# Performance work log

Hardware: AMD Instinct MI355X
Metric: run time of the kernel (lower is better)

Reference implementation:

```python
import jax, jax.numpy as jnp
import numpy as np

N = 50000        # nodes
E = 800000       # edges
D_IN = 128       # input feature dim
HID = 64         # hidden_dim
HEADS = 4
OUT = 2          # output_dim (fraud / not-fraud)
BN_EPS = 1e-5
NEG_SLOPE = 0.2  # PyG GATv2Conv default


def setup_inputs() -> dict:
    key = jax.random.key(0)
    ks = jax.random.split(key, 16)
    g = lambda k, shape, s=0.05: (jax.random.normal(k, shape, jnp.float32) * s)
    HC = HEADS * HID  # 256
    return {
        "x": jax.random.normal(ks[0], (N, D_IN), jnp.float32),
        "edge_index": jax.random.randint(ks[1], (2, E), 0, N),
        # input projection
        "W_in": g(ks[2], (D_IN, HID)), "b_in": jnp.zeros((HID,), jnp.float32),
        # GATv2 layer 0: HID -> HID, 4 heads (concat -> 256)
        "Wl0": g(ks[3], (HID, HC)), "Wr0": g(ks[4], (HID, HC)),
        "att0": g(ks[5], (HEADS, HID)), "bias0": jnp.zeros((HC,), jnp.float32),
        # GATv2 layer 1: 256 -> HID, 4 heads (concat -> 256)
        "Wl1": g(ks[6], (HC, HC)), "Wr1": g(ks[7], (HC, HC)),
        "att1": g(ks[8], (HEADS, HID)), "bias1": jnp.zeros((HC,), jnp.float32),
        # GATv2 layer 2: 256 -> OUT, 1 head
        "Wl2": g(ks[9], (HC, OUT)), "Wr2": g(ks[10], (HC, OUT)),
        "att2": g(ks[11], (1, OUT)), "bias2": jnp.zeros((OUT,), jnp.float32),
        # BatchNorm (eval mode: running stats) for the first num_layers-1 = 2 layers
        "bn_gamma": jnp.ones((2, HC), jnp.float32),
        "bn_beta": jnp.zeros((2, HC), jnp.float32),
        "bn_mean": jnp.zeros((2, HC), jnp.float32),
        "bn_var": jnp.ones((2, HC), jnp.float32),
    }


def _gatv2(h, src, dst, Wl, Wr, att, bias):
    """PyG GATv2Conv (concat=True, negative_slope=0.2). src->dst messages."""
    n = h.shape[0]
    heads, c = att.shape
    xl = (h @ Wl).reshape(n, heads, c)   # source transform
    xr = (h @ Wr).reshape(n, heads, c)   # target transform
    e = jax.nn.leaky_relu(xl[src] + xr[dst], NEG_SLOPE)       # [E, H, C]
    logits = jnp.einsum('ehc,hc->eh', e, att)                 # [E, H]
    # segment softmax over incoming edges of each destination node
    m = jax.ops.segment_max(logits, dst, num_segments=n)      # [N, H]
    ex = jnp.exp(logits - m[dst])
    denom = jax.ops.segment_sum(ex, dst, num_segments=n)
    alpha = ex / denom[dst]                                   # [E, H]
    out = jax.ops.segment_sum(xl[src] * alpha[..., None], dst, num_segments=n)
    return out.reshape(n, heads * c) + bias


def _bn_eval(h, gamma, beta, mean, var):
    return gamma * (h - mean) * jax.lax.rsqrt(var + BN_EPS) + beta


def reference(x, edge_index, W_in, b_in, Wl0, Wr0, att0, bias0,
              Wl1, Wr1, att1, bias1, Wl2, Wr2, att2, bias2,
              bn_gamma, bn_beta, bn_mean, bn_var):
    n = x.shape[0]
    loop = jnp.arange(n)
    src = jnp.concatenate([edge_index[0], loop])  # PyG add_self_loops=True
    dst = jnp.concatenate([edge_index[1], loop])

    h = jax.nn.relu(x @ W_in + b_in)              # dropout is identity in eval

    # layer 0 (no residual: 64 != 256)
    h = _gatv2(h, src, dst, Wl0, Wr0, att0, bias0)
    h = jax.nn.relu(_bn_eval(h, bn_gamma[0], bn_beta[0], bn_mean[0], bn_var[0]))

    # layer 1 (residual: 256 == 256)
    h_prev = h
    h = _gatv2(h, src, dst, Wl1, Wr1, att1, bias1)
    h = jax.nn.relu(_bn_eval(h, bn_gamma[1], bn_beta[1], bn_mean[1], bn_var[1]))
    h = h + h_prev

    # output layer, 1 head
    h = _gatv2(h, src, dst, Wl2, Wr2, att2, bias2)
    return jax.nn.log_softmax(h, axis=1)
```

## Files before the change

kernel.cpp:

```cpp
#include <hip/hip_runtime.h>
#include <hip/hip_bf16.h>
#include <math.h>


using h16     = _Float16;
using half2v  = __attribute__((ext_vector_type(2))) h16;
using half4v  = __attribute__((ext_vector_type(4))) h16;
using half8   = __attribute__((ext_vector_type(8))) h16;
using floatx4 = __attribute__((ext_vector_type(4))) float;

__device__ __forceinline__ float lrelu(float x) { return x > 0.f ? x : 0.2f * x; }

__device__ __forceinline__ half2v shfl_xor_h2(half2v v, int mask) {
    float f = __builtin_bit_cast(float, v);
    f = __shfl_xor(f, mask, 64);
    return __builtin_bit_cast(half2v, f);
}

__global__ void zero_int(int* __restrict__ p, int n) {
    int t = blockIdx.x * blockDim.x + threadIdx.x;
    if (t < n) p[t] = 0;
}

__global__ void hist_dst(const int* __restrict__ ei, int E, int* __restrict__ deg) {
    int e = blockIdx.x * blockDim.x + threadIdx.x;
    if (e < E) atomicAdd(&deg[ei[E + e]], 1);
}

__global__ __launch_bounds__(256) void scan_blk(const int* __restrict__ deg,
                                                int* __restrict__ rowstart,
                                                int* __restrict__ bsum, int N) {
    int t = blockIdx.x * 256 + threadIdx.x;
    int lane = threadIdx.x & 63, wid = threadIdx.x >> 6;
    int v = (t < N) ? deg[t] : 0;
    int x = v;
#pragma unroll
    for (int off = 1; off < 64; off <<= 1) {
        int y = __shfl_up(x, off, 64);
        if (lane >= off) x += y;
    }
    __shared__ int wsum[4];
    if (lane == 63) wsum[wid] = x;
    __syncthreads();
    int add = 0;
#pragma unroll
    for (int w = 0; w < 4; ++w) if (w < wid) add += wsum[w];
    int incl = x + add;
    if (t < N) rowstart[t] = incl - v;
    if (threadIdx.x == 255) bsum[blockIdx.x] = incl;
}

__global__ __launch_bounds__(256) void scan_off(int* __restrict__ bsum, int NB) {
    int t = threadIdx.x;
    int lane = t & 63, wid = t >> 6;
    int v = (t < NB) ? bsum[t] : 0;
    int x = v;
#pragma unroll
    for (int off = 1; off < 64; off <<= 1) {
        int y = __shfl_up(x, off, 64);
        if (lane >= off) x += y;
    }
    __shared__ int wsum[4];
    if (lane == 63) wsum[wid] = x;
    __syncthreads();
    int add = 0;
#pragma unroll
    for (int w = 0; w < 4; ++w) if (w < wid) add += wsum[w];
    if (t < NB) bsum[t] = x + add - v;
}

__global__ void add_off(const int* __restrict__ bsum, int* __restrict__ rowstart,
                        int* __restrict__ cursor, int N) {
    int t = blockIdx.x * 256 + threadIdx.x;
    if (t >= N) return;
    int r = rowstart[t] + bsum[blockIdx.x];
    rowstart[t] = r;
    cursor[t] = r;
}

__global__ void scatter_src(const int* __restrict__ ei, int E,
                            int* __restrict__ cursor, int* __restrict__ csr_src) {
    int e = blockIdx.x * blockDim.x + threadIdx.x;
    if (e >= E) return;
    int d = ei[E + e];
    int pos = atomicAdd(&cursor[d], 1);
    csr_src[pos] = ei[e];
}

__device__ __forceinline__ void pack_one(const float* __restrict__ W,
                                         h16* __restrict__ Wp,
                                         int t, int K, int NC) {
    int j = t & 7;
    int l = (t >> 3) & 63;
    int rest = t >> 9;
    int NT = NC >> 4;
    int nt = rest % NT;
    int kc = rest / NT;
    int row = kc * 32 + (l >> 4) * 8 + j;
    int col = nt * 16 + (l & 15);
    Wp[t] = (h16)W[(size_t)row * NC + col];
}

__global__ void pack_all(const float* __restrict__ W_in,
                         const float* __restrict__ Wl0, const float* __restrict__ Wr0,
                         const float* __restrict__ Wl1, const float* __restrict__ Wr1,
                         h16* __restrict__ P_in,
                         h16* __restrict__ P_l0, h16* __restrict__ P_r0,
                         h16* __restrict__ P_l1, h16* __restrict__ P_r1,
                         const float4* __restrict__ x, half4v* __restrict__ xh, int n4) {
    int t = blockIdx.x * blockDim.x + threadIdx.x;
    if (t < 8192)        pack_one(W_in, P_in, t, 128, 64);
    else if (t < 24576)  pack_one(Wl0, P_l0, t - 8192, 64, 256);
    else if (t < 40960)  pack_one(Wr0, P_r0, t - 24576, 64, 256);
    else if (t < 106496) pack_one(Wl1, P_l1, t - 40960, 256, 256);
    else if (t < 172032) pack_one(Wr1, P_r1, t - 106496, 256, 256);
    else {
        int u = t - 172032;
        if (u < n4) {
            float4 v = x[u];
            half4v o = { (h16)v.x, (h16)v.y, (h16)v.z, (h16)v.w };
            xh[u] = o;
        }
    }
}

template<int KC, int NT, bool RELU, bool DUAL>
__global__ __launch_bounds__(256) void gemm_lds(
        const h16* __restrict__ Xh,
        const h16* __restrict__ Wp0, const h16* __restrict__ Wp1,
        const float* __restrict__ bias,
        h16* __restrict__ out0, h16* __restrict__ out1, int M) {
    constexpr int K = KC * 32;
    constexpr int ldo = NT * 16;
    constexpr int CHUNK8 = NT * 64;
    constexpr int PER_THR = CHUNK8 / 256;
    __shared__ half8 wbuf[2][CHUNK8];

    const h16* Wp = (DUAL && blockIdx.y) ? Wp1 : Wp0;
    h16* out = (DUAL && blockIdx.y) ? out1 : out0;
    const half8* WG = (const half8*)Wp;

    const int tid = threadIdx.x;
    const int wid = tid >> 6, lane = tid & 63;
    const int quad = lane >> 4, li = lane & 15;
    const int r0 = blockIdx.x * 64 + wid * 16;
    int arow = r0 + li; if (arow >= M) arow = M - 1;
    const half8* A8 = (const half8*)Xh + (size_t)arow * (K / 8) + quad;

    floatx4 acc[NT];
#pragma unroll
    for (int t = 0; t < NT; ++t) acc[t] = (floatx4){0.f, 0.f, 0.f, 0.f};

    half8 st[PER_THR];
#pragma unroll
    for (int i = 0; i < PER_THR; ++i) st[i] = WG[i * 256 + tid];
#pragma unroll
    for (int i = 0; i < PER_THR; ++i) wbuf[0][i * 256 + tid] = st[i];
    __syncthreads();

#pragma unroll
    for (int kc = 0; kc < KC; ++kc) {
        int cur = kc & 1;
        if (kc + 1 < KC) {
#pragma unroll
            for (int i = 0; i < PER_THR; ++i)
                st[i] = WG[(size_t)(kc + 1) * CHUNK8 + i * 256 + tid];
        }
        half8 a = A8[kc * 4];
#pragma unroll
        for (int nt = 0; nt < NT; ++nt) {
            half8 b = wbuf[cur][nt * 64 + lane];
            acc[nt] = __builtin_amdgcn_mfma_f32_16x16x32_f16(a, b, acc[nt], 0, 0, 0);
        }
        if (kc + 1 < KC) {
#pragma unroll
            for (int i = 0; i < PER_THR; ++i) wbuf[cur ^ 1][i * 256 + tid] = st[i];
        }
        __syncthreads();
    }

#pragma unroll
    for (int nt = 0; nt < NT; ++nt) {
#pragma unroll
        for (int reg = 0; reg < 4; ++reg) {
            int rr = r0 + quad * 4 + reg;
            if (rr >= M) continue;
            float v = acc[nt][reg];
            if (RELU) v = fmaxf(v + bias[nt * 16 + li], 0.f);
            out[(size_t)rr * ldo + nt * 16 + li] = (h16)v;
        }
    }
}

__global__ void attn4_bn(int N, const h16* __restrict__ XL, const h16* __restrict__ XR,
                         const float* __restrict__ att,
                         const int* __restrict__ rowstart, const int* __restrict__ deg,
                         const int* __restrict__ csr_src,
                         const float* __restrict__ gamma, const float* __restrict__ beta,
                         const float* __restrict__ mean, const float* __restrict__ var,
                         const float* __restrict__ bias, const float* __restrict__ resid,
                         float* __restrict__ out, h16* __restrict__ outb) {
    int d = blockIdx.x * (blockDim.x >> 6) + (threadIdx.x >> 6);
    int lane = threadIdx.x & 63;
    if (d >= N) return;
    half4v bv = *(const half4v*)(XR + (size_t)d * 256 + lane * 4);
    float4 wf = ((const float4*)att)[lane];
    half2v b0 = bv.xy, b1 = bv.zw;
    half2v w0 = { (h16)wf.x, (h16)wf.y };
    half2v w1 = { (h16)wf.z, (h16)wf.w };
    const h16 k02 = (h16)0.2f;

    auto edge_part = [&](half4v xv) -> h16 {
        half2v e0 = xv.xy + b0, e1 = xv.zw + b1;
        half2v l0 = __builtin_elementwise_max(e0, e0 * k02);
        half2v l1 = __builtin_elementwise_max(e1, e1 * k02);
        half2v qd = l0 * w0 + l1 * w1;
        return qd.x + qd.y;
    };

    half4v av = *(const half4v*)(XL + (size_t)d * 256 + lane * 4);
    float p = (float)edge_part(av);
    p += __shfl_xor(p, 1, 64); p += __shfl_xor(p, 2, 64);
    p += __shfl_xor(p, 4, 64); p += __shfl_xor(p, 8, 64);
    float es = __expf(p);
    float l = es;
    float4 acc = { es * (float)av.x, es * (float)av.y, es * (float)av.z, es * (float)av.w };

    int start = rowstart[d], n = deg[d];
    for (int i = 0; i < n; i += 4) {
        int nm1 = n - 1;
        int s0 = csr_src[start + i];
        int s1 = csr_src[start + min(i + 1, nm1)];
        int s2 = csr_src[start + min(i + 2, nm1)];
        int s3 = csr_src[start + min(i + 3, nm1)];
        half4v x0 = *(const half4v*)(XL + (size_t)s0 * 256 + lane * 4);
        half4v x1 = *(const half4v*)(XL + (size_t)s1 * 256 + lane * 4);
        half4v x2 = *(const half4v*)(XL + (size_t)s2 * 256 + lane * 4);
        half4v x3 = *(const half4v*)(XL + (size_t)s3 * 256 + lane * 4);
        half2v p01 = { edge_part(x0), edge_part(x1) };
        half2v p23 = { edge_part(x2), edge_part(x3) };
#pragma unroll
        for (int s = 1; s < 16; s <<= 1) {
            p01 += shfl_xor_h2(p01, s);
            p23 += shfl_xor_h2(p23, s);
        }
        int rem = n - i;
        float e0 = __expf((float)p01.x);
        float e1 = (rem > 1) ? __expf((float)p01.y) : 0.f;
        float e2 = (rem > 2) ? __expf((float)p23.x) : 0.f;
        float e3 = (rem > 3) ? __expf((float)p23.y) : 0.f;
        l += (e0 + e1) + (e2 + e3);
        acc.x += e0 * (float)x0.x + e1 * (float)x1.x + e2 * (float)x2.x + e3 * (float)x3.x;
        acc.y += e0 * (float)x0.y + e1 * (float)x1.y + e2 * (float)x2.y + e3 * (float)x3.y;
        acc.z += e0 * (float)x0.z + e1 * (float)x1.z + e2 * (float)x2.z + e3 * (float)x3.z;
        acc.w += e0 * (float)x0.w + e1 * (float)x1.w + e2 * (float)x2.w + e3 * (float)x3.w;
    }
    float inv = 1.f / l;
    float4 g  = ((const float4*)gamma)[lane];
    float4 be = ((const float4*)beta)[lane];
    float4 mu = ((const float4*)mean)[lane];
    float4 va = ((const float4*)var)[lane];
    float4 bi = ((const float4*)bias)[lane];
    float4 sc4, sh4;
    sc4.x = g.x * rsqrtf(va.x + 1e-5f); sh4.x = (bi.x - mu.x) * sc4.x + be.x;
    sc4.y = g.y * rsqrtf(va.y + 1e-5f); sh4.y = (bi.y - mu.y) * sc4.y + be.y;
    sc4.z = g.z * rsqrtf(va.z + 1e-5f); sh4.z = (bi.z - mu.z) * sc4.z + be.z;
    sc4.w = g.w * rsqrtf(va.w + 1e-5f); sh4.w = (bi.w - mu.w) * sc4.w + be.w;
    float4 o;
    o.x = fmaxf(acc.x * inv * sc4.x + sh4.x, 0.f);
    o.y = fmaxf(acc.y * inv * sc4.y + sh4.y, 0.f);
    o.z = fmaxf(acc.z * inv * sc4.z + sh4.z, 0.f);
    o.w = fmaxf(acc.w * inv * sc4.w + sh4.w, 0.f);
    if (resid) {
        float4 rv = *(const float4*)(resid + (size_t)d * 256 + lane * 4);
        o.x += rv.x; o.y += rv.y; o.z += rv.z; o.w += rv.w;
    }
    *(float4*)(out + (size_t)d * 256 + lane * 4) = o;
    if (outb) {
        half4v ob = { (h16)o.x, (h16)o.y, (h16)o.z, (h16)o.w };
        *(half4v*)(outb + (size_t)d * 256 + lane * 4) = ob;
    }
}

__global__ void gemm2_wave(const float* __restrict__ X, const float* __restrict__ Wl,
                           const float* __restrict__ Wr, float* __restrict__ xl2,
                           float* __restrict__ xr2, int N) {
    int t = blockIdx.x * blockDim.x + threadIdx.x;
    int n = t >> 4;
    int sl = t & 15;
    if (n >= N) return;
    const float4* Xr = (const float4*)(X + (size_t)n * 256);
    const float4* Wl4 = (const float4*)Wl;
    const float4* Wr4 = (const float4*)Wr;
    float l0 = 0.f, l1 = 0.f, r0 = 0.f, r1 = 0.f;
#pragma unroll
    for (int j = 0; j < 4; ++j) {
        int idx = sl + j * 16;
        float4 xv = Xr[idx];
        float4 wa = Wl4[idx * 2];
        float4 wb = Wl4[idx * 2 + 1];
        l0 += xv.x * wa.x + xv.y * wa.z + xv.z * wb.x + xv.w * wb.z;
        l1 += xv.x * wa.y + xv.y * wa.w + xv.z * wb.y + xv.w * wb.w;
        wa = Wr4[idx * 2]; wb = Wr4[idx * 2 + 1];
        r0 += xv.x * wa.x + xv.y * wa.z + xv.z * wb.x + xv.w * wb.z;
        r1 += xv.x * wa.y + xv.y * wa.w + xv.z * wb.y + xv.w * wb.w;
    }
#pragma unroll
    for (int off = 1; off < 16; off <<= 1) {
        l0 += __shfl_xor(l0, off, 64);
        l1 += __shfl_xor(l1, off, 64);
        r0 += __shfl_xor(r0, off, 64);
        r1 += __shfl_xor(r1, off, 64);
    }
    if (sl == 0) {
        xl2[n * 2] = l0; xl2[n * 2 + 1] = l1;
        xr2[n * 2] = r0; xr2[n * 2 + 1] = r1;
    }
}

__global__ void attn1_16(int N, const float* __restrict__ xl2, const float* __restrict__ xr2,
                         const float* __restrict__ att, const float* __restrict__ bias,
                         const int* __restrict__ rowstart, const int* __restrict__ deg,
                         const int* __restrict__ csr_src, float* __restrict__ out) {
    int t = blockIdx.x * blockDim.x + threadIdx.x;
    int d = t >> 4, sl = t & 15;
    if (d >= N) return;
    float a0 = att[0], a1 = att[1];
    float2 xr = ((const float2*)xr2)[d];
    float b0 = xr.x, b1 = xr.y;
    float l = 0.f, ac0 = 0.f, ac1 = 0.f;
    int st = rowstart[d], n = deg[d];
    if (sl == 0) {
        float2 s = ((const float2*)xl2)[d];
        float p = lrelu(s.x + b0) * a0 + lrelu(s.y + b1) * a1;
        float e = __expf(p);
        l = e; ac0 = e * s.x; ac1 = e * s.y;
    }
    for (int i = sl; i < n; i += 16) {
        int s = csr_src[st + i];
        float2 xv = ((const float2*)xl2)[s];
        float q = lrelu(xv.x + b0) * a0 + lrelu(xv.y + b1) * a1;
        float e = __expf(q);
        l += e; ac0 += e * xv.x; ac1 += e * xv.y;
    }
#pragma unroll
    for (int off = 1; off < 16; off <<= 1) {
        l   += __shfl_xor(l, off, 64);
        ac0 += __shfl_xor(ac0, off, 64);
        ac1 += __shfl_xor(ac1, off, 64);
    }
    if (sl == 0) {
        float inv = 1.f / l;
        float v0 = ac0 * inv + bias[0];
        float v1 = ac1 * inv + bias[1];
        float mx = fmaxf(v0, v1);
        float lse = mx + logf(__expf(v0 - mx) + __expf(v1 - mx));
        out[d * 2] = v0 - lse;
        out[d * 2 + 1] = v1 - lse;
    }
}

extern "C" void kernel_launch(void* const* d_in, const int* in_sizes, int n_in,
                              void* d_out, int out_size, void* d_ws, size_t ws_size,
                              hipStream_t stream) {
    const float* x        = (const float*)d_in[0];
    const int*   ei       = (const int*)  d_in[1];
    const float* W_in     = (const float*)d_in[2];
    const float* b_in     = (const float*)d_in[3];
    const float* Wl0      = (const float*)d_in[4];
    const float* Wr0      = (const float*)d_in[5];
    const float* att0     = (const float*)d_in[6];
    const float* bias0    = (const float*)d_in[7];
    const float* Wl1      = (const float*)d_in[8];
    const float* Wr1      = (const float*)d_in[9];
    const float* att1     = (const float*)d_in[10];
    const float* bias1    = (const float*)d_in[11];
    const float* Wl2      = (const float*)d_in[12];
    const float* Wr2      = (const float*)d_in[13];
    const float* att2     = (const float*)d_in[14];
    const float* bias2    = (const float*)d_in[15];
    const float* bn_gamma = (const float*)d_in[16];
    const float* bn_beta  = (const float*)d_in[17];
    const float* bn_mean  = (const float*)d_in[18];
    const float* bn_var   = (const float*)d_in[19];

    const int N  = in_sizes[0] / 128;
    const int E  = in_sizes[1] / 2;
    const int NB = (N + 255) / 256;

    float* ws = (float*)d_ws;
    size_t off = 0;
    float* C    = ws + off; off += (size_t)N * 256;
    float* D    = ws + off; off += (size_t)N * 256;
    float* XL2  = ws + off; off += (size_t)N * 2;
    float* XR2  = ws + off; off += (size_t)N * 2;
    h16* Ah   = (h16*)(ws + off); off += (size_t)N * 128;
    h16* Bh   = (h16*)(ws + off); off += (size_t)N * 128;
    h16* Ch   = (h16*)(ws + off); off += (size_t)N * 128;
    h16* H0h  = (h16*)(ws + off); off += (size_t)N * 32;
    h16* xh   = (h16*)(ws + off); off += (size_t)N * 64;
    h16* Wp_in = (h16*)(ws + off); off += 4096;
    h16* Wp_l0 = (h16*)(ws + off); off += 8192;
    h16* Wp_r0 = (h16*)(ws + off); off += 8192;
    h16* Wp_l1 = (h16*)(ws + off); off += 32768;
    h16* Wp_r1 = (h16*)(ws + off); off += 32768;
    int* ip = (int*)(ws + off);
    int* deg      = ip;              ip += N;
    int* rowstart = ip;              ip += N;
    int* cursor   = ip;              ip += N;
    int* bsum     = ip;              ip += NB;
    int* csr_src  = ip;              ip += E;

    zero_int<<<(N + 255) / 256, 256, 0, stream>>>(deg, N);
    hist_dst<<<(E + 255) / 256, 256, 0, stream>>>(ei, E, deg);
    scan_blk<<<NB, 256, 0, stream>>>(deg, rowstart, bsum, N);
    scan_off<<<1, 256, 0, stream>>>(bsum, NB);
    add_off<<<NB, 256, 0, stream>>>(bsum, rowstart, cursor, N);
    scatter_src<<<(E + 255) / 256, 256, 0, stream>>>(ei, E, cursor, csr_src);

    pack_all<<<(172032 + N * 32 + 255) / 256, 256, 0, stream>>>(
        W_in, Wl0, Wr0, Wl1, Wr1, Wp_in, Wp_l0, Wp_r0, Wp_l1, Wp_r1,
        (const float4*)x, (half4v*)xh, N * 32);

    const int GBM = (N + 63) / 64;

    gemm_lds<4, 4, true, false><<<GBM, 256, 0, stream>>>(
        xh, Wp_in, nullptr, b_in, H0h, nullptr, N);

    gemm_lds<2, 16, false, true><<<dim3(GBM, 2), 256, 0, stream>>>(
        H0h, Wp_l0, Wp_r0, nullptr, Ah, Bh, N);
    attn4_bn<<<(N + 3) / 4, 256, 0, stream>>>(N, Ah, Bh, att0, rowstart, deg, csr_src,
                                              bn_gamma, bn_beta, bn_mean, bn_var,
                                              bias0, nullptr, C, Ch);

    gemm_lds<8, 16, false, true><<<dim3(GBM, 2), 256, 0, stream>>>(
        Ch, Wp_l1, Wp_r1, nullptr, Ah, Bh, N);
    attn4_bn<<<(N + 3) / 4, 256, 0, stream>>>(N, Ah, Bh, att1, rowstart, deg, csr_src,
                                              bn_gamma + 256, bn_beta + 256, bn_mean + 256,
                                              bn_var + 256, bias1, C, D, nullptr);

    gemm2_wave<<<(N * 16 + 255) / 256, 256, 0, stream>>>(D, Wl2, Wr2, XL2, XR2, N);
    attn1_16<<<(N * 16 + 255) / 256, 256, 0, stream>>>(N, XL2, XR2, att2, bias2,
                                                       rowstart, deg, csr_src, (float*)d_out);
}
```

Before: 438.3 us.

## Use fp16 accumulation in attention, fp16 layer-1 output, fuse deg zeroing, prefetch indices

The attention aggregation now accumulates messages in packed half2 arithmetic instead of fp32 and software-prefetches the next group of CSR source indices while the current features load. The layer-1 attention output is written only as fp16 (Dh), so the fp32 buffer D disappears and gemm2_wave reads half the bytes. Zeroing the degree array moves into the pack_all kernel, removing one launch. fp16 accumulation over high-degree nodes risks precision loss or overflow of unnormalized exp-weighted sums.

```diff
diff --git a/kernel.cpp b/kernel.cpp
--- a/kernel.cpp
+++ b/kernel.cpp
@@ -15,11 +15,6 @@
     float f = __builtin_bit_cast(float, v);
     f = __shfl_xor(f, mask, 64);
     return __builtin_bit_cast(half2v, f);
-}
-
-__global__ void zero_int(int* __restrict__ p, int n) {
-    int t = blockIdx.x * blockDim.x + threadIdx.x;
-    if (t < n) p[t] = 0;
 }
 
 __global__ void hist_dst(const int* __restrict__ ei, int E, int* __restrict__ deg) {
@@ -107,20 +102,22 @@
                          h16* __restrict__ P_in,
                          h16* __restrict__ P_l0, h16* __restrict__ P_r0,
                          h16* __restrict__ P_l1, h16* __restrict__ P_r1,
-                         const float4* __restrict__ x, half4v* __restrict__ xh, int n4) {
+                         const float4* __restrict__ x, half4v* __restrict__ xh, int n4,
+                         int* __restrict__ deg, int N) {
     int t = blockIdx.x * blockDim.x + threadIdx.x;
     if (t < 8192)        pack_one(W_in, P_in, t, 128, 64);
     else if (t < 24576)  pack_one(Wl0, P_l0, t - 8192, 64, 256);
     else if (t < 40960)  pack_one(Wr0, P_r0, t - 24576, 64, 256);
     else if (t < 106496) pack_one(Wl1, P_l1, t - 40960, 256, 256);
     else if (t < 172032) pack_one(Wr1, P_r1, t - 106496, 256, 256);
-    else {
+    else if (t < 172032 + n4) {
         int u = t - 172032;
-        if (u < n4) {
-            float4 v = x[u];
-            half4v o = { (h16)v.x, (h16)v.y, (h16)v.z, (h16)v.w };
-            xh[u] = o;
-        }
+        float4 v = x[u];
+        half4v o = { (h16)v.x, (h16)v.y, (h16)v.z, (h16)v.w };
+        xh[u] = o;
+    } else {
+        int u = t - 172032 - n4;
+        if (u < N) deg[u] = 0;
     }
 }
 
@@ -224,19 +221,33 @@
     p += __shfl_xor(p, 4, 64); p += __shfl_xor(p, 8, 64);
     float es = __expf(p);
     float l = es;
-    float4 acc = { es * (float)av.x, es * (float)av.y, es * (float)av.z, es * (float)av.w };
+    h16 eh = (h16)es;
+    half2v ebc = { eh, eh };
+    half2v acc0 = ebc * av.xy;
+    half2v acc1 = ebc * av.zw;
 
     int start = rowstart[d], n = deg[d];
+    int nm1 = n - 1;
+    int t0 = 0, t1 = 0, t2 = 0, t3 = 0;
+    if (n > 0) {
+        t0 = csr_src[start];
+        t1 = csr_src[start + min(1, nm1)];
+        t2 = csr_src[start + min(2, nm1)];
+        t3 = csr_src[start + min(3, nm1)];
+    }
     for (int i = 0; i < n; i += 4) {
-        int nm1 = n - 1;
-        int s0 = csr_src[start + i];
-        int s1 = csr_src[start + min(i + 1, nm1)];
-        int s2 = csr_src[start + min(i + 2, nm1)];
-        int s3 = csr_src[start + min(i + 3, nm1)];
+        int s0 = t0, s1 = t1, s2 = t2, s3 = t3;
         half4v x0 = *(const half4v*)(XL + (size_t)s0 * 256 + lane * 4);
         half4v x1 = *(const half4v*)(XL + (size_t)s1 * 256 + lane * 4);
         half4v x2 = *(const half4v*)(XL + (size_t)s2 * 256 + lane * 4);
         half4v x3 = *(const half4v*)(XL + (size_t)s3 * 256 + lane * 4);
+        int j = i + 4;
+        if (j < n) {
+            t0 = csr_src[start + j];
+            t1 = csr_src[start + min(j + 1, nm1)];
+            t2 = csr_src[start + min(j + 2, nm1)];
+            t3 = csr_src[start + min(j + 3, nm1)];
+        }
         half2v p01 = { edge_part(x0), edge_part(x1) };
         half2v p23 = { edge_part(x2), edge_part(x3) };
 #pragma unroll
@@ -250,11 +261,14 @@
         float e2 = (rem > 2) ? __expf((float)p23.x) : 0.f;
         float e3 = (rem > 3) ? __expf((float)p23.y) : 0.f;
         l += (e0 + e1) + (e2 + e3);
-        acc.x += e0 * (float)x0.x + e1 * (float)x1.x + e2 * (float)x2.x + e3 * (float)x3.x;
-        acc.y += e0 * (float)x0.y + e1 * (float)x1.y + e2 * (float)x2.y + e3 * (float)x3.y;
-        acc.z += e0 * (float)x0.z + e1 * (float)x1.z + e2 * (float)x2.z + e3 * (float)x3.z;
-        acc.w += e0 * (float)x0.w + e1 * (float)x1.w + e2 * (float)x2.w + e3 * (float)x3.w;
-    }
+        h16 h0 = (h16)e0, h1 = (h16)e1, h2 = (h16)e2, h3 = (h16)e3;
+        half2v eb0 = { h0, h0 }, eb1 = { h1, h1 }, eb2 = { h2, h2 }, eb3 = { h3, h3 };
+        acc0 += eb0 * x0.xy; acc1 += eb0 * x0.zw;
+        acc0 += eb1 * x1.xy; acc1 += eb1 * x1.zw;
+        acc0 += eb2 * x2.xy; acc1 += eb2 * x2.zw;
+        acc0 += eb3 * x3.xy; acc1 += eb3 * x3.zw;
+    }
+    float4 acc = { (float)acc0.x, (float)acc0.y, (float)acc1.x, (float)acc1.y };
     float inv = 1.f / l;
     float4 g  = ((const float4*)gamma)[lane];
     float4 be = ((const float4*)beta)[lane];
@@ -275,28 +289,29 @@
         float4 rv = *(const float4*)(resid + (size_t)d * 256 + lane * 4);
         o.x += rv.x; o.y += rv.y; o.z += rv.z; o.w += rv.w;
     }
-    *(float4*)(out + (size_t)d * 256 + lane * 4) = o;
+    if (out) *(float4*)(out + (size_t)d * 256 + lane * 4) = o;
     if (outb) {
         half4v ob = { (h16)o.x, (h16)o.y, (h16)o.z, (h16)o.w };
         *(half4v*)(outb + (size_t)d * 256 + lane * 4) = ob;
     }
 }
 
-__global__ void gemm2_wave(const float* __restrict__ X, const float* __restrict__ Wl,
+__global__ void gemm2_wave(const h16* __restrict__ X, const float* __restrict__ Wl,
                            const float* __restrict__ Wr, float* __restrict__ xl2,
                            float* __restrict__ xr2, int N) {
     int t = blockIdx.x * blockDim.x + threadIdx.x;
     int n = t >> 4;
     int sl = t & 15;
     if (n >= N) return;
-    const float4* Xr = (const float4*)(X + (size_t)n * 256);
+    const half4v* Xr = (const half4v*)(X + (size_t)n * 256);
     const float4* Wl4 = (const float4*)Wl;
     const float4* Wr4 = (const float4*)Wr;
     float l0 = 0.f, l1 = 0.f, r0 = 0.f, r1 = 0.f;
 #pragma unroll
     for (int j = 0; j < 4; ++j) {
         int idx = sl + j * 16;
-        float4 xv = Xr[idx];
+        half4v xh = Xr[idx];
+        float4 xv = { (float)xh.x, (float)xh.y, (float)xh.z, (float)xh.w };
         float4 wa = Wl4[idx * 2];
         float4 wb = Wl4[idx * 2 + 1];
         l0 += xv.x * wa.x + xv.y * wa.z + xv.z * wb.x + xv.w * wb.z;
@@ -391,12 +406,12 @@
     float* ws = (float*)d_ws;
     size_t off = 0;
     float* C    = ws + off; off += (size_t)N * 256;
-    float* D    = ws + off; off += (size_t)N * 256;
     float* XL2  = ws + off; off += (size_t)N * 2;
     float* XR2  = ws + off; off += (size_t)N * 2;
     h16* Ah   = (h16*)(ws + off); off += (size_t)N * 128;
     h16* Bh   = (h16*)(ws + off); off += (size_t)N * 128;
     h16* Ch   = (h16*)(ws + off); off += (size_t)N * 128;
+    h16* Dh   = (h16*)(ws + off); off += (size_t)N * 128;
     h16* H0h  = (h16*)(ws + off); off += (size_t)N * 32;
     h16* xh   = (h16*)(ws + off); off += (size_t)N * 64;
     h16* Wp_in = (h16*)(ws + off); off += 4096;
@@ -411,17 +426,17 @@
     int* bsum     = ip;              ip += NB;
     int* csr_src  = ip;              ip += E;
 
-    zero_int<<<(N + 255) / 256, 256, 0, stream>>>(deg, N);
+    const int PACK_T = 172032 + N * 32 + N;
+    pack_all<<<(PACK_T + 255) / 256, 256, 0, stream>>>(
+        W_in, Wl0, Wr0, Wl1, Wr1, Wp_in, Wp_l0, Wp_r0, Wp_l1, Wp_r1,
+        (const float4*)x, (half4v*)xh, N * 32, deg, N);
+
     hist_dst<<<(E + 255) / 256, 256, 0, stream>>>(ei, E, deg);
     scan_blk<<<NB, 256, 0, stream>>>(deg, rowstart, bsum, N);
     scan_off<<<1, 256, 0, stream>>>(bsum, NB);
     add_off<<<NB, 256, 0, stream>>>(bsum, rowstart, cursor, N);
     scatter_src<<<(E + 255) / 256, 256, 0, stream>>>(ei, E, cursor, csr_src);
 
-    pack_all<<<(172032 + N * 32 + 255) / 256, 256, 0, stream>>>(
-        W_in, Wl0, Wr0, Wl1, Wr1, Wp_in, Wp_l0, Wp_r0, Wp_l1, Wp_r1,
-        (const float4*)x, (half4v*)xh, N * 32);
-
     const int GBM = (N + 63) / 64;
 
     gemm_lds<4, 4, true, false><<<GBM, 256, 0, stream>>>(
@@ -437,9 +452,9 @@
         Ch, Wp_l1, Wp_r1, nullptr, Ah, Bh, N);
     attn4_bn<<<(N + 3) / 4, 256, 0, stream>>>(N, Ah, Bh, att1, rowstart, deg, csr_src,
                                               bn_gamma + 256, bn_beta + 256, bn_mean + 256,
-                                              bn_var + 256, bias1, C, D, nullptr);
-
-    gemm2_wave<<<(N * 16 + 255) / 256, 256, 0, stream>>>(D, Wl2, Wr2, XL2, XR2, N);
+                                              bn_var + 256, bias1, C, nullptr, Dh);
+
+    gemm2_wave<<<(N * 16 + 255) / 256, 256, 0, stream>>>(Dh, Wl2, Wr2, XL2, XR2, N);
     attn1_16<<<(N * 16 + 255) / 256, 256, 0, stream>>>(N, XL2, XR2, att2, bias2,
                                                        rowstart, deg, csr_src, (float*)d_out);
 }
```

Result: faster. 418.9 us (-4.4%).
